# Performance work log

Hardware: AMD Instinct MI355X
Metric: run time of the kernel (lower is better)

Reference implementation:

```python
import jax, jax.numpy as jnp
import numpy as np

EPS_LN = 1e-5

def _ln(x, w, b):
    m = x.mean(-1, keepdims=True)
    v = x.var(-1, keepdims=True)  # biased var, matching torch LayerNorm
    return (x - m) / jnp.sqrt(v + EPS_LN) * w + b


def setup_inputs() -> dict:
    key = jax.random.key(0)
    ks = jax.random.split(key, 20)
    B, N, C = 8, 4096, 256
    def lin_w(k, i, o):
        return (jax.random.normal(k, (i, o), jnp.float32) / np.sqrt(i)).astype(jnp.float32)
    inp = {
        'xyz': jax.random.normal(ks[0], (B, N, 3), jnp.float32),
        'features': jax.random.normal(ks[1], (B, N, C), jnp.float32),
        # geo_mlp: Linear(10,32), LN(32), ReLU, Linear(32,16)
        'g_w1': lin_w(ks[2], 10, 32), 'g_b1': jnp.zeros((32,), jnp.float32),
        'g_lnw': jnp.ones((32,), jnp.float32), 'g_lnb': jnp.zeros((32,), jnp.float32),
        'g_w2': lin_w(ks[3], 32, 16), 'g_b2': jnp.zeros((16,), jnp.float32),
        # edge_pred: Linear(C+16,64), LN(64), ReLU, Linear(64,1), Sigmoid
        'e_w1': lin_w(ks[4], C + 16, 64), 'e_b1': jnp.zeros((64,), jnp.float32),
        'e_lnw': jnp.ones((64,), jnp.float32), 'e_lnb': jnp.zeros((64,), jnp.float32),
        'e_w2': lin_w(ks[5], 64, 1), 'e_b2': jnp.zeros((1,), jnp.float32),
        # edge_refine: Linear(C,C), LN(C), ReLU
        'r_w': lin_w(ks[6], C, C), 'r_b': jnp.zeros((C,), jnp.float32),
        'r_lnw': jnp.ones((C,), jnp.float32), 'r_lnb': jnp.zeros((C,), jnp.float32),
    }
    return inp


def reference(xyz, features, g_w1, g_b1, g_lnw, g_lnb, g_w2, g_b2,
              e_w1, e_b1, e_lnw, e_lnb, e_w2, e_b2, r_w, r_b, r_lnw, r_lnb):
    k = 16
    # KNN: pairwise negative squared distance, top-k largest = nearest
    sq = jnp.sum(xyz * xyz, axis=-1)                              # [B,N]
    pd = 2.0 * jnp.einsum('bnd,bmd->bnm', xyz, xyz) - sq[:, :, None] - sq[:, None, :]
    idx = jax.lax.top_k(pd, k)[1]                                 # [B,N,k]
    nbr = jax.vmap(lambda p, i: p[i])(xyz, idx)                   # [B,N,k,3]
    cen = nbr - nbr.mean(axis=2, keepdims=True)                   # centered neighborhoods
    cov = jnp.einsum('bnkc,bnkd->bncd', cen, cen) / k             # [B,N,3,3]
    trace = cov[..., 0, 0] + cov[..., 1, 1] + cov[..., 2, 2]
    det = jnp.clip(cov[..., 0, 0] * cov[..., 1, 1] * cov[..., 2, 2], 1e-8, None)
    std = jnp.std(cen, axis=2, ddof=1)                            # [B,N,3] (torch unbiased std)
    d = jnp.linalg.norm(cen, axis=3)                              # [B,N,k]
    mean_d = d.mean(axis=2)
    std_d = jnp.std(d, axis=2, ddof=1)
    t = trace + 1e-6
    geo = jnp.stack([trace, det, std[..., 0], std[..., 1], std[..., 2],
                     mean_d, std_d, std[..., 0] / t, std[..., 1] / t, std[..., 2] / t], axis=-1)
    geo = jax.nn.relu(_ln(geo @ g_w1 + g_b1, g_lnw, g_lnb)) @ g_w2 + g_b2    # [B,N,16]
    comb = jnp.concatenate([features, geo], axis=-1)
    edge_prob = jax.nn.sigmoid(jax.nn.relu(_ln(comb @ e_w1 + e_b1, e_lnw, e_lnb)) @ e_w2 + e_b2)
    refined = jax.nn.relu(_ln(features @ r_w + r_b, r_lnw, r_lnb))
    refined = features + refined * edge_prob
    return refined, edge_prob
```

## Files before the change

kernel.cpp:

```cpp
#include <hip/hip_runtime.h>
#include <math.h>

#define BATCH 8
#define NPTS  4096
#define CF    256
#define TOPK  16
#define TOTQ  (BATCH*NPTS)
#define EPOFF ((size_t)TOTQ*CF)

__global__ __launch_bounds__(256) void prep_xyz_k(const float* __restrict__ xyz,
                                                  float4* __restrict__ tab) {
    int i = blockIdx.x*256 + threadIdx.x;
    if (i < TOTQ) {
        float x = xyz[3*i], y = xyz[3*i+1], z = xyz[3*i+2];
        tab[i] = make_float4(x, y, z, x*x + y*y + z*z);
    }
}

__global__ __launch_bounds__(256, 2) void knn_geo_k(
    const float4* __restrict__ tab,
    const float* __restrict__ g_w1, const float* __restrict__ g_b1,
    const float* __restrict__ g_lnw, const float* __restrict__ g_lnb,
    const float* __restrict__ g_w2, const float* __restrict__ g_b2,
    float* __restrict__ geo_out)
{
    __shared__ float2 lst[TOPK][256];
    __shared__ float4 coords[64][TOPK+1];
    __shared__ float s_w1[320], s_b1[32], s_lnw[32], s_lnb[32], s_w2[512], s_b2[16];

    const int tid = threadIdx.x;
    for (int v = tid; v < 320; v += 256) s_w1[v] = g_w1[v];
    for (int v = tid; v < 512; v += 256) s_w2[v] = g_w2[v];
    if (tid < 32) { s_b1[tid] = g_b1[tid]; s_lnw[tid] = g_lnw[tid]; s_lnb[tid] = g_lnb[tid]; }
    if (tid < 16) s_b2[tid] = g_b2[tid];

    const int ql = tid & 63;
    const int qg = blockIdx.x*64 + ql;
    const int b  = blockIdx.x >> 6;
    const float4* __restrict__ ctab = tab + b*NPTS;
    const int ibase = __builtin_amdgcn_readfirstlane((tid >> 6) << 10);

    float4 q4 = tab[qg];
    const float qx = q4.x, qy = q4.y, qz = q4.z, qs = q4.w;

    float vals[TOPK]; int idxs[TOPK];
    #pragma unroll
    for (int j = 0; j < TOPK; ++j) { vals[j] = -INFINITY; idxs[j] = 0; }
    int   cnt = 0;
    float thr = -INFINITY;

    auto flushbuf = [&]() {
        for (int e = 0; e < cnt; ++e) {
            float2 en = lst[e][tid];
            float pv = en.x;
            int   pj = __float_as_int(en.y);
            if (pv > vals[TOPK-1]) {
                #pragma unroll
                for (int j = TOPK-1; j >= 1; --j) {
                    bool shift = pv > vals[j-1];
                    bool place = (!shift) && (pv > vals[j]);
                    vals[j] = shift ? vals[j-1] : (place ? pv : vals[j]);
                    idxs[j] = shift ? idxs[j-1] : (place ? pj : idxs[j]);
                }
                if (pv > vals[0]) { vals[0] = pv; idxs[0] = pj; }
            }
        }
    };

    float4 cbuf[8];
    #pragma unroll
    for (int u = 0; u < 8; ++u) cbuf[u] = ctab[ibase + u];

    for (int ib = 0; ib < 1024; ib += 8) {
        float4 cur[8];
        #pragma unroll
        for (int u = 0; u < 8; ++u) cur[u] = cbuf[u];
        if (ib + 8 < 1024) {
            #pragma unroll
            for (int u = 0; u < 8; ++u) cbuf[u] = ctab[ibase + ib + 8 + u];
        }
        #pragma unroll
        for (int u = 0; u < 8; ++u) {
            float dot = fmaf(qx, cur[u].x, fmaf(qy, cur[u].y, qz*cur[u].z));
            float pd  = fmaf(2.f, dot, -(qs + cur[u].w));
            if (pd > thr) {
                lst[cnt][tid] = make_float2(pd, __int_as_float(ibase + ib + u));
                ++cnt;
            }
        }
        if (__any(cnt > 8)) { flushbuf(); cnt = 0; thr = vals[TOPK-1]; }
    }
    flushbuf();

    #pragma unroll
    for (int e = 0; e < TOPK; ++e)
        lst[e][tid] = make_float2(vals[e], __int_as_float(idxs[e]));
    __syncthreads();

    if (tid < 64) {
        const int q = tid;
        int p0 = 0, p1 = 0, p2 = 0, p3 = 0;
        float sx = 0, sy = 0, sz = 0;
        for (int r = 0; r < TOPK; ++r) {
            float2 h0 = lst[p0][q];
            float2 h1 = lst[p1][64 + q];
            float2 h2 = lst[p2][128 + q];
            float2 h3 = lst[p3][192 + q];
            float best = h0.x; int bj = __float_as_int(h0.y); int bs = 0;
            if (h1.x > best) { best = h1.x; bj = __float_as_int(h1.y); bs = 1; }
            if (h2.x > best) { best = h2.x; bj = __float_as_int(h2.y); bs = 2; }
            if (h3.x > best) { best = h3.x; bj = __float_as_int(h3.y); bs = 3; }
            p0 += (bs == 0); p1 += (bs == 1); p2 += (bs == 2); p3 += (bs == 3);
            float4 nb = ctab[bj];
            coords[q][r] = nb;
            sx += nb.x; sy += nb.y; sz += nb.z;
        }
        const float mx = sx/16.f, my = sy/16.f, mz = sz/16.f;
        float sxx = 0, syy = 0, szz = 0, sd = 0;
        float dist[TOPK];
        #pragma unroll
        for (int r = 0; r < TOPK; ++r) {
            float4 nb = coords[q][r];
            float cx = nb.x - mx, cy = nb.y - my, cz = nb.z - mz;
            sxx += cx*cx; syy += cy*cy; szz += cz*cz;
            float dd = sqrtf(cx*cx + cy*cy + cz*cz);
            dist[r] = dd; sd += dd;
        }
        const float md = sd/16.f;
        float sdd = 0;
        #pragma unroll
        for (int r = 0; r < TOPK; ++r) { float t = dist[r] - md; sdd += t*t; }
        const float c00 = sxx/16.f, c11 = syy/16.f, c22 = szz/16.f;
        const float trace = c00 + c11 + c22;
        const float det = fmaxf(c00*c11*c22, 1e-8f);
        const float s0 = sqrtf(sxx/15.f), s1 = sqrtf(syy/15.f), s2 = sqrtf(szz/15.f);
        const float stdd = sqrtf(sdd/15.f);
        const float tt = trace + 1e-6f;
        float geo[10] = {trace, det, s0, s1, s2, md, stdd, s0/tt, s1/tt, s2/tt};

        float z1[32];
        #pragma unroll
        for (int jj = 0; jj < 32; ++jj) {
            float a = s_b1[jj];
            #pragma unroll
            for (int i = 0; i < 10; ++i) a = fmaf(geo[i], s_w1[i*32 + jj], a);
            z1[jj] = a;
        }
        float mzn = 0;
        #pragma unroll
        for (int jj = 0; jj < 32; ++jj) mzn += z1[jj];
        mzn /= 32.f;
        float vz = 0;
        #pragma unroll
        for (int jj = 0; jj < 32; ++jj) { float t = z1[jj] - mzn; vz += t*t; }
        vz /= 32.f;
        const float rs = 1.f/sqrtf(vz + 1e-5f);
        float h[32];
        #pragma unroll
        for (int jj = 0; jj < 32; ++jj)
            h[jj] = fmaxf((z1[jj]-mzn)*rs*s_lnw[jj] + s_lnb[jj], 0.f);
        float og[16];
        #pragma unroll
        for (int c = 0; c < 16; ++c) {
            float a = s_b2[c];
            #pragma unroll
            for (int i = 0; i < 32; ++i) a = fmaf(h[i], s_w2[i*16 + c], a);
            og[c] = a;
        }
        float4* gout = (float4*)(geo_out + (size_t)qg*16);
        gout[0] = make_float4(og[0],  og[1],  og[2],  og[3]);
        gout[1] = make_float4(og[4],  og[5],  og[6],  og[7]);
        gout[2] = make_float4(og[8],  og[9],  og[10], og[11]);
        gout[3] = make_float4(og[12], og[13], og[14], og[15]);
    }
}

__global__ __launch_bounds__(256, 2) void edge_k(
    const float* __restrict__ feat, const float* __restrict__ geo16,
    const float* __restrict__ e_w1, const float* __restrict__ e_b1,
    const float* __restrict__ e_lnw, const float* __restrict__ e_lnb,
    const float* __restrict__ e_w2, const float* __restrict__ e_b2,
    const float* __restrict__ r_w,  const float* __restrict__ r_b,
    const float* __restrict__ r_lnw, const float* __restrict__ r_lnb,
    float* __restrict__ out)
{
    __shared__ float fl[32*260];
    __shared__ float wb[4096];
    __shared__ float gl[512];

    const int tid = threadIdx.x;
    const int pbase = blockIdx.x*32;

    {
        const float4* f4 = (const float4*)(feat + (size_t)pbase*CF);
        #pragma unroll
        for (int k = 0; k < 8; ++k) {
            int v = tid + k*256;
            float4 x = f4[v];
            *(float4*)&fl[(v >> 6)*260 + (v & 63)*4] = x;
        }
        if (tid < 128) {
            float4 x = ((const float4*)(geo16 + (size_t)pbase*16))[tid];
            *(float4*)&gl[(tid >> 2)*16 + (tid & 3)*4] = x;
        }
    }
    __syncthreads();

    const int pq = tid >> 4, cq = tid & 15;
    const int p0 = pq*2, p1 = p0 + 1;

    float a0[4] = {0,0,0,0}, a1[4] = {0,0,0,0};
    for (int kc = 0; kc < 256; kc += 64) {
        __syncthreads();
        #pragma unroll
        for (int k = 0; k < 4; ++k) {
            int v = tid + k*256;
            *(float4*)&wb[(v >> 4)*64 + (v & 15)*4] =
                *(const float4*)&e_w1[(size_t)(kc + (v >> 4))*64 + (v & 15)*4];
        }
        __syncthreads();
        #pragma unroll 8
        for (int k = 0; k < 64; ++k) {
            float f0 = fl[p0*260 + kc + k];
            float f1 = fl[p1*260 + kc + k];
            float4 w = *(float4*)&wb[k*64 + cq*4];
            a0[0] = fmaf(f0, w.x, a0[0]); a0[1] = fmaf(f0, w.y, a0[1]);
            a0[2] = fmaf(f0, w.z, a0[2]); a0[3] = fmaf(f0, w.w, a0[3]);
            a1[0] = fmaf(f1, w.x, a1[0]); a1[1] = fmaf(f1, w.y, a1[1]);
            a1[2] = fmaf(f1, w.z, a1[2]); a1[3] = fmaf(f1, w.w, a1[3]);
        }
    }
    __syncthreads();
    {
        int v = tid;
        *(float4*)&wb[(v >> 4)*64 + (v & 15)*4] =
            *(const float4*)&e_w1[(size_t)(256 + (v >> 4))*64 + (v & 15)*4];
    }
    __syncthreads();
    #pragma unroll
    for (int k = 0; k < 16; ++k) {
        float f0 = gl[p0*16 + k];
        float f1 = gl[p1*16 + k];
        float4 w = *(float4*)&wb[k*64 + cq*4];
        a0[0] = fmaf(f0, w.x, a0[0]); a0[1] = fmaf(f0, w.y, a0[1]);
        a0[2] = fmaf(f0, w.z, a0[2]); a0[3] = fmaf(f0, w.w, a0[3]);
        a1[0] = fmaf(f1, w.x, a1[0]); a1[1] = fmaf(f1, w.y, a1[1]);
        a1[2] = fmaf(f1, w.z, a1[2]); a1[3] = fmaf(f1, w.w, a1[3]);
    }
    {
        float4 bb = *(const float4*)&e_b1[cq*4];
        a0[0]+=bb.x; a0[1]+=bb.y; a0[2]+=bb.z; a0[3]+=bb.w;
        a1[0]+=bb.x; a1[1]+=bb.y; a1[2]+=bb.z; a1[3]+=bb.w;
    }
    float s0 = a0[0]+a0[1]+a0[2]+a0[3];
    float s1 = a1[0]+a1[1]+a1[2]+a1[3];
    #pragma unroll
    for (int sw = 1; sw < 16; sw <<= 1) { s0 += __shfl_xor(s0, sw); s1 += __shfl_xor(s1, sw); }
    const float m0 = s0/64.f, m1 = s1/64.f;
    float v0 = 0, v1 = 0;
    #pragma unroll
    for (int j = 0; j < 4; ++j) { float t0 = a0[j]-m0, t1 = a1[j]-m1; v0 += t0*t0; v1 += t1*t1; }
    #pragma unroll
    for (int sw = 1; sw < 16; sw <<= 1) { v0 += __shfl_xor(v0, sw); v1 += __shfl_xor(v1, sw); }
    const float r0 = 1.f/sqrtf(v0/64.f + 1e-5f);
    const float r1 = 1.f/sqrtf(v1/64.f + 1e-5f);
    float4 lw = *(const float4*)&e_lnw[cq*4];
    float4 lb = *(const float4*)&e_lnb[cq*4];
    float4 w2 = *(const float4*)&e_w2[cq*4];
    float d0 = 0, d1 = 0;
    {
        float hh;
        hh = fmaxf((a0[0]-m0)*r0*lw.x + lb.x, 0.f); d0 = fmaf(hh, w2.x, d0);
        hh = fmaxf((a0[1]-m0)*r0*lw.y + lb.y, 0.f); d0 = fmaf(hh, w2.y, d0);
        hh = fmaxf((a0[2]-m0)*r0*lw.z + lb.z, 0.f); d0 = fmaf(hh, w2.z, d0);
        hh = fmaxf((a0[3]-m0)*r0*lw.w + lb.w, 0.f); d0 = fmaf(hh, w2.w, d0);
        hh = fmaxf((a1[0]-m1)*r1*lw.x + lb.x, 0.f); d1 = fmaf(hh, w2.x, d1);
        hh = fmaxf((a1[1]-m1)*r1*lw.y + lb.y, 0.f); d1 = fmaf(hh, w2.y, d1);
        hh = fmaxf((a1[2]-m1)*r1*lw.z + lb.z, 0.f); d1 = fmaf(hh, w2.z, d1);
        hh = fmaxf((a1[3]-m1)*r1*lw.w + lb.w, 0.f); d1 = fmaf(hh, w2.w, d1);
    }
    #pragma unroll
    for (int sw = 1; sw < 16; sw <<= 1) { d0 += __shfl_xor(d0, sw); d1 += __shfl_xor(d1, sw); }
    const float eb2 = e_b2[0];
    const float ep0 = 1.f/(1.f + expf(-(d0 + eb2)));
    const float ep1 = 1.f/(1.f + expf(-(d1 + eb2)));
    if (cq == 0) {
        out[EPOFF + pbase + p0] = ep0;
        out[EPOFF + pbase + p1] = ep1;
    }

    float b0[4][4], b1v[4][4];
    #pragma unroll
    for (int o = 0; o < 4; ++o)
        #pragma unroll
        for (int j = 0; j < 4; ++j) { b0[o][j] = 0.f; b1v[o][j] = 0.f; }

    for (int kc = 0; kc < 256; kc += 16) {
        __syncthreads();
        #pragma unroll
        for (int k = 0; k < 8; ++k) {
            int v = tid + k*256;
            *(float4*)&wb[(v >> 6)*256 + (v & 63)*4] =
                *(const float4*)&r_w[(size_t)(kc + (v >> 6))*256 + (v & 63)*4];
        }
        __syncthreads();
        #pragma unroll
        for (int k = 0; k < 16; ++k) {
            float f0 = fl[p0*260 + kc + k];
            float f1 = fl[p1*260 + kc + k];
            #pragma unroll
            for (int o = 0; o < 4; ++o) {
                float4 w = *(float4*)&wb[k*256 + o*64 + cq*4];
                b0[o][0] = fmaf(f0, w.x, b0[o][0]); b0[o][1] = fmaf(f0, w.y, b0[o][1]);
                b0[o][2] = fmaf(f0, w.z, b0[o][2]); b0[o][3] = fmaf(f0, w.w, b0[o][3]);
                b1v[o][0] = fmaf(f1, w.x, b1v[o][0]); b1v[o][1] = fmaf(f1, w.y, b1v[o][1]);
                b1v[o][2] = fmaf(f1, w.z, b1v[o][2]); b1v[o][3] = fmaf(f1, w.w, b1v[o][3]);
            }
        }
    }
    #pragma unroll
    for (int o = 0; o < 4; ++o) {
        float4 rb = *(const float4*)&r_b[o*64 + cq*4];
        b0[o][0]+=rb.x; b0[o][1]+=rb.y; b0[o][2]+=rb.z; b0[o][3]+=rb.w;
        b1v[o][0]+=rb.x; b1v[o][1]+=rb.y; b1v[o][2]+=rb.z; b1v[o][3]+=rb.w;
    }
    float S0 = 0, S1 = 0;
    #pragma unroll
    for (int o = 0; o < 4; ++o)
        #pragma unroll
        for (int j = 0; j < 4; ++j) { S0 += b0[o][j]; S1 += b1v[o][j]; }
    #pragma unroll
    for (int sw = 1; sw < 16; sw <<= 1) { S0 += __shfl_xor(S0, sw); S1 += __shfl_xor(S1, sw); }
    const float M0 = S0/256.f, M1 = S1/256.f;
    float V0 = 0, V1 = 0;
    #pragma unroll
    for (int o = 0; o < 4; ++o)
        #pragma unroll
        for (int j = 0; j < 4; ++j) {
            float t0 = b0[o][j]-M0, t1 = b1v[o][j]-M1;
            V0 += t0*t0; V1 += t1*t1;
        }
    #pragma unroll
    for (int sw = 1; sw < 16; sw <<= 1) { V0 += __shfl_xor(V0, sw); V1 += __shfl_xor(V1, sw); }
    const float R0 = 1.f/sqrtf(V0/256.f + 1e-5f);
    const float R1 = 1.f/sqrtf(V1/256.f + 1e-5f);

    #pragma unroll
    for (int o = 0; o < 4; ++o) {
        float4 lw4 = *(const float4*)&r_lnw[o*64 + cq*4];
        float4 lb4 = *(const float4*)&r_lnb[o*64 + cq*4];
        float4 f0v = *(float4*)&fl[p0*260 + o*64 + cq*4];
        float4 f1v = *(float4*)&fl[p1*260 + o*64 + cq*4];
        float4 o0, o1;
        o0.x = f0v.x + fmaxf((b0[o][0]-M0)*R0*lw4.x + lb4.x, 0.f)*ep0;
        o0.y = f0v.y + fmaxf((b0[o][1]-M0)*R0*lw4.y + lb4.y, 0.f)*ep0;
        o0.z = f0v.z + fmaxf((b0[o][2]-M0)*R0*lw4.z + lb4.z, 0.f)*ep0;
        o0.w = f0v.w + fmaxf((b0[o][3]-M0)*R0*lw4.w + lb4.w, 0.f)*ep0;
        o1.x = f1v.x + fmaxf((b1v[o][0]-M1)*R1*lw4.x + lb4.x, 0.f)*ep1;
        o1.y = f1v.y + fmaxf((b1v[o][1]-M1)*R1*lw4.y + lb4.y, 0.f)*ep1;
        o1.z = f1v.z + fmaxf((b1v[o][2]-M1)*R1*lw4.z + lb4.z, 0.f)*ep1;
        o1.w = f1v.w + fmaxf((b1v[o][3]-M1)*R1*lw4.w + lb4.w, 0.f)*ep1;
        *(float4*)&out[((size_t)(pbase + p0))*CF + o*64 + cq*4] = o0;
        *(float4*)&out[((size_t)(pbase + p1))*CF + o*64 + cq*4] = o1;
    }
}

extern "C" void kernel_launch(void* const* d_in, const int* in_sizes, int n_in,
                              void* d_out, int out_size, void* d_ws, size_t ws_size,
                              hipStream_t stream) {
    (void)in_sizes; (void)n_in; (void)out_size; (void)ws_size;
    const float* xyz   = (const float*)d_in[0];
    const float* feat  = (const float*)d_in[1];
    const float* g_w1  = (const float*)d_in[2];
    const float* g_b1  = (const float*)d_in[3];
    const float* g_lnw = (const float*)d_in[4];
    const float* g_lnb = (const float*)d_in[5];
    const float* g_w2  = (const float*)d_in[6];
    const float* g_b2  = (const float*)d_in[7];
    const float* e_w1  = (const float*)d_in[8];
    const float* e_b1  = (const float*)d_in[9];
    const float* e_lnw = (const float*)d_in[10];
    const float* e_lnb = (const float*)d_in[11];
    const float* e_w2  = (const float*)d_in[12];
    const float* e_b2  = (const float*)d_in[13];
    const float* r_w   = (const float*)d_in[14];
    const float* r_b   = (const float*)d_in[15];
    const float* r_lnw = (const float*)d_in[16];
    const float* r_lnb = (const float*)d_in[17];
    float* out = (float*)d_out;

    float*  geo_ws = (float*)d_ws;
    float4* tab    = (float4*)((char*)d_ws + (size_t)TOTQ*16*sizeof(float));

    hipLaunchKernelGGL(prep_xyz_k, dim3(TOTQ/256), dim3(256), 0, stream, xyz, tab);
    hipLaunchKernelGGL(knn_geo_k, dim3(TOTQ/64), dim3(256), 0, stream,
                       tab, g_w1, g_b1, g_lnw, g_lnb, g_w2, g_b2, geo_ws);
    hipLaunchKernelGGL(edge_k, dim3(TOTQ/32), dim3(256), 0, stream,
                       feat, geo_ws, e_w1, e_b1, e_lnw, e_lnb, e_w2, e_b2,
                       r_w, r_b, r_lnw, r_lnb, out);
}
```

Baseline: 344.9 us.

## Move edge/refine GEMMs to bf16x3 MFMA with pre-split pre-swizzled weights

Replaces the scalar FP32 FMA matmuls in edge_k with MFMA 16x16x32 bf16 instructions. Each operand is split into a high and a low bf16 part, and three products are summed to keep close to FP32 accuracy. A new prep kernel converts and swizzles r_w and e_w1 into MFMA-friendly layouts each call. The weights are streamed into LDS with global_load_lds double buffering, and the block is widened to 64 points. LayerNorm statistics switch to a one-pass sum/sum-of-squares form, which adds some numerical risk. The larger LDS footprint drops occupancy to one block per CU.

```diff
diff --git a/kernel.cpp b/kernel.cpp
--- a/kernel.cpp
+++ b/kernel.cpp
@@ -8,12 +8,53 @@
 #define TOTQ  (BATCH*NPTS)
 #define EPOFF ((size_t)TOTQ*CF)
 
+typedef __attribute__((ext_vector_type(8))) short bf16x8;
+typedef __attribute__((ext_vector_type(4))) float f32x4;
+
+__device__ __forceinline__ unsigned short f2bf(float x) {
+    union { float f; unsigned u; } a; a.f = x;
+    unsigned r = a.u + 0x7fffu + ((a.u >> 16) & 1u);
+    return (unsigned short)(r >> 16);
+}
+__device__ __forceinline__ float bf2f(unsigned short h) {
+    union { float f; unsigned u; } a; a.u = ((unsigned)h) << 16; return a.f;
+}
+__device__ __forceinline__ void gl_lds16(const void* g, void* l) {
+    __builtin_amdgcn_global_load_lds(
+        (const __attribute__((address_space(1))) unsigned int*)g,
+        (__attribute__((address_space(3))) unsigned int*)l, 16, 0, 0);
+}
+
 __global__ __launch_bounds__(256) void prep_xyz_k(const float* __restrict__ xyz,
                                                   float4* __restrict__ tab) {
     int i = blockIdx.x*256 + threadIdx.x;
     if (i < TOTQ) {
         float x = xyz[3*i], y = xyz[3*i+1], z = xyz[3*i+2];
         tab[i] = make_float4(x, y, z, x*x + y*y + z*z);
+    }
+}
+
+__global__ __launch_bounds__(256) void prep_w_k(
+    const float* __restrict__ rw, const float* __restrict__ ew1,
+    unsigned short* __restrict__ rwh, unsigned short* __restrict__ rwl,
+    unsigned short* __restrict__ ewh, unsigned short* __restrict__ ewl)
+{
+    int t = blockIdx.x*256 + threadIdx.x;
+    if (t < 65536) {
+        int k = t >> 8, n = t & 255;
+        float x = rw[t];
+        unsigned short h = f2bf(x);
+        unsigned short l = f2bf(x - bf2f(h));
+        int dst = (((k>>5)*16 + (n>>4)) << 9) + ((k>>3)&3)*128 + (n&15)*8 + (k&7);
+        rwh[dst] = h; rwl[dst] = l;
+    }
+    if (t < 288*64) {
+        int k = t >> 6, n = t & 63;
+        float x = (k < 272) ? ew1[k*64 + n] : 0.f;
+        unsigned short h = f2bf(x);
+        unsigned short l = f2bf(x - bf2f(h));
+        int dst = (((k>>5)*4 + (n>>4)) << 9) + ((k>>3)&3)*128 + (n&15)*8 + (k&7);
+        ewh[dst] = h; ewl[dst] = l;
     }
 }
 
@@ -175,193 +216,273 @@
     }
 }
 
-__global__ __launch_bounds__(256, 2) void edge_k(
+__global__ __launch_bounds__(256, 1) void edge_k(
     const float* __restrict__ feat, const float* __restrict__ geo16,
-    const float* __restrict__ e_w1, const float* __restrict__ e_b1,
-    const float* __restrict__ e_lnw, const float* __restrict__ e_lnb,
-    const float* __restrict__ e_w2, const float* __restrict__ e_b2,
-    const float* __restrict__ r_w,  const float* __restrict__ r_b,
-    const float* __restrict__ r_lnw, const float* __restrict__ r_lnb,
+    const unsigned short* __restrict__ rwh, const unsigned short* __restrict__ rwl,
+    const unsigned short* __restrict__ ewh, const unsigned short* __restrict__ ewl,
+    const float* __restrict__ e_b1, const float* __restrict__ e_lnw,
+    const float* __restrict__ e_lnb, const float* __restrict__ e_w2,
+    const float* __restrict__ e_b2,
+    const float* __restrict__ r_b, const float* __restrict__ r_lnw,
+    const float* __restrict__ r_lnb,
     float* __restrict__ out)
 {
-    __shared__ float fl[32*260];
-    __shared__ float wb[4096];
-    __shared__ float gl[512];
-
-    const int tid = threadIdx.x;
-    const int pbase = blockIdx.x*32;
-
+    __shared__ unsigned short sAh[64*296];
+    __shared__ unsigned short sAl[64*296];
+    __shared__ unsigned char  sB[65536];
+    __shared__ float s_eb1[64], s_elnw[64], s_elnb[64], s_ew2[64];
+    __shared__ float s_rb[256], s_rlnw[256], s_rlnb[256];
+    __shared__ float s_ep[64], s_m[64], s_rs[64];
+    __shared__ float sPx[256], sPq[256];
+
+    const int tid  = threadIdx.x;
+    const int lane = tid & 63;
+    const int wv   = tid >> 6;
+    const int lr   = lane & 15;
+    const int lg   = lane >> 4;
+    const int pbase = blockIdx.x * 64;
+
+    if (tid < 64) { s_eb1[tid]=e_b1[tid]; s_elnw[tid]=e_lnw[tid]; s_elnb[tid]=e_lnb[tid]; s_ew2[tid]=e_w2[tid]; }
+    s_rb[tid]=r_b[tid]; s_rlnw[tid]=r_lnw[tid]; s_rlnb[tid]=r_lnb[tid];
+
+    const float4* f4 = (const float4*)(feat + (size_t)pbase*CF);
+    #pragma unroll
+    for (int it = 0; it < 16; ++it) {
+        int v = tid + it*256;
+        float4 x = f4[v];
+        int row = v >> 6, c0 = (v & 63)*4;
+        unsigned short h0=f2bf(x.x), h1=f2bf(x.y), h2=f2bf(x.z), h3=f2bf(x.w);
+        unsigned short l0=f2bf(x.x-bf2f(h0)), l1=f2bf(x.y-bf2f(h1));
+        unsigned short l2=f2bf(x.z-bf2f(h2)), l3=f2bf(x.w-bf2f(h3));
+        *(ushort4*)&sAh[row*296 + c0] = make_ushort4(h0,h1,h2,h3);
+        *(ushort4*)&sAl[row*296 + c0] = make_ushort4(l0,l1,l2,l3);
+    }
     {
-        const float4* f4 = (const float4*)(feat + (size_t)pbase*CF);
-        #pragma unroll
-        for (int k = 0; k < 8; ++k) {
-            int v = tid + k*256;
-            float4 x = f4[v];
-            *(float4*)&fl[(v >> 6)*260 + (v & 63)*4] = x;
-        }
-        if (tid < 128) {
-            float4 x = ((const float4*)(geo16 + (size_t)pbase*16))[tid];
-            *(float4*)&gl[(tid >> 2)*16 + (tid & 3)*4] = x;
-        }
-    }
+        const float4* g4 = (const float4*)(geo16 + (size_t)pbase*16);
+        float4 x = g4[tid];
+        int row = tid >> 2, c0 = 256 + (tid & 3)*4;
+        unsigned short h0=f2bf(x.x), h1=f2bf(x.y), h2=f2bf(x.z), h3=f2bf(x.w);
+        unsigned short l0=f2bf(x.x-bf2f(h0)), l1=f2bf(x.y-bf2f(h1));
+        unsigned short l2=f2bf(x.z-bf2f(h2)), l3=f2bf(x.w-bf2f(h3));
+        *(ushort4*)&sAh[row*296 + c0] = make_ushort4(h0,h1,h2,h3);
+        *(ushort4*)&sAl[row*296 + c0] = make_ushort4(l0,l1,l2,l3);
+        int zc = 272 + (tid & 3)*4;
+        *(ushort4*)&sAh[row*296 + zc] = make_ushort4(0,0,0,0);
+        *(ushort4*)&sAl[row*296 + zc] = make_ushort4(0,0,0,0);
+    }
+
+    auto stage3 = [&](int c, int buf) {
+        const char* sh = (const char*)rwh + c*16384;
+        const char* sl = (const char*)rwl + c*16384;
+        char* dh = (char*)sB + buf*32768;
+        char* dl = dh + 16384;
+        #pragma unroll
+        for (int i = 0; i < 4; ++i) {
+            gl_lds16(sh + i*4096 + wv*1024 + lane*16, dh + i*4096 + wv*1024);
+            gl_lds16(sl + i*4096 + wv*1024 + lane*16, dl + i*4096 + wv*1024);
+        }
+    };
+    auto stage2 = [&](int c, int buf) {
+        const char* sh = (const char*)ewh + c*4096;
+        const char* sl = (const char*)ewl + c*4096;
+        char* d = (char*)sB + 32768 + buf*8192;
+        gl_lds16(sh + wv*1024 + lane*16, d + wv*1024);
+        gl_lds16(sl + wv*1024 + lane*16, d + 4096 + wv*1024);
+    };
+
+    stage2(0, 0);
+    stage3(0, 0);
     __syncthreads();
 
-    const int pq = tid >> 4, cq = tid & 15;
-    const int p0 = pq*2, p1 = p0 + 1;
-
-    float a0[4] = {0,0,0,0}, a1[4] = {0,0,0,0};
-    for (int kc = 0; kc < 256; kc += 64) {
+    f32x4 acc2[4];
+    #pragma unroll
+    for (int i = 0; i < 4; ++i) acc2[i] = (f32x4){0.f,0.f,0.f,0.f};
+    const int arow2 = (wv*16 + lr)*296;
+    for (int c = 0; c < 9; ++c) {
+        if (c < 8) stage2(c+1, (c+1)&1);
+        bf16x8 ah = *(const bf16x8*)&sAh[arow2 + c*32 + lg*8];
+        bf16x8 al = *(const bf16x8*)&sAl[arow2 + c*32 + lg*8];
+        const unsigned short* bb = (const unsigned short*)(sB + 32768 + (c&1)*8192);
+        #pragma unroll
+        for (int nt = 0; nt < 4; ++nt) {
+            bf16x8 bh = *(const bf16x8*)&bb[nt*512 + lane*8];
+            bf16x8 bl = *(const bf16x8*)&bb[2048 + nt*512 + lane*8];
+            acc2[nt] = __builtin_amdgcn_mfma_f32_16x16x32_bf16(al, bh, acc2[nt], 0,0,0);
+            acc2[nt] = __builtin_amdgcn_mfma_f32_16x16x32_bf16(ah, bl, acc2[nt], 0,0,0);
+            acc2[nt] = __builtin_amdgcn_mfma_f32_16x16x32_bf16(ah, bh, acc2[nt], 0,0,0);
+        }
         __syncthreads();
-        #pragma unroll
-        for (int k = 0; k < 4; ++k) {
-            int v = tid + k*256;
-            *(float4*)&wb[(v >> 4)*64 + (v & 15)*4] =
-                *(const float4*)&e_w1[(size_t)(kc + (v >> 4))*64 + (v & 15)*4];
+    }
+
+    {
+        float px[4] = {0,0,0,0}, pq[4] = {0,0,0,0};
+        #pragma unroll
+        for (int nt = 0; nt < 4; ++nt) {
+            float bv = s_eb1[nt*16 + lr];
+            #pragma unroll
+            for (int j = 0; j < 4; ++j) {
+                acc2[nt][j] += bv;
+                px[j] += acc2[nt][j];
+                pq[j] += acc2[nt][j]*acc2[nt][j];
+            }
+        }
+        #pragma unroll
+        for (int sw = 1; sw < 16; sw <<= 1) {
+            #pragma unroll
+            for (int j = 0; j < 4; ++j) { px[j] += __shfl_xor(px[j], sw); pq[j] += __shfl_xor(pq[j], sw); }
+        }
+        float mj[4], rj[4], dd[4] = {0,0,0,0};
+        #pragma unroll
+        for (int j = 0; j < 4; ++j) {
+            mj[j] = px[j]*(1.f/64.f);
+            float var = pq[j]*(1.f/64.f) - mj[j]*mj[j];
+            rj[j] = rsqrtf(var + 1e-5f);
+        }
+        #pragma unroll
+        for (int nt = 0; nt < 4; ++nt) {
+            int col = nt*16 + lr;
+            float lw = s_elnw[col], lb = s_elnb[col], w2 = s_ew2[col];
+            #pragma unroll
+            for (int j = 0; j < 4; ++j) {
+                float h = fmaxf((acc2[nt][j]-mj[j])*rj[j]*lw + lb, 0.f);
+                dd[j] = fmaf(h, w2, dd[j]);
+            }
+        }
+        #pragma unroll
+        for (int sw = 1; sw < 16; sw <<= 1) {
+            #pragma unroll
+            for (int j = 0; j < 4; ++j) dd[j] += __shfl_xor(dd[j], sw);
+        }
+        float eb2v = e_b2[0];
+        #pragma unroll
+        for (int j = 0; j < 4; ++j) {
+            if (lr == j) {
+                int row = wv*16 + lg*4 + j;
+                float ep = 1.f/(1.f + expf(-(dd[j] + eb2v)));
+                s_ep[row] = ep;
+                out[EPOFF + pbase + row] = ep;
+            }
+        }
+    }
+
+    f32x4 acc3[4][4];
+    #pragma unroll
+    for (int mt = 0; mt < 4; ++mt)
+        #pragma unroll
+        for (int nt = 0; nt < 4; ++nt) acc3[mt][nt] = (f32x4){0.f,0.f,0.f,0.f};
+
+    for (int c = 0; c < 8; ++c) {
+        if (c < 7) stage3(c+1, (c+1)&1);
+        bf16x8 ah[4], al[4];
+        #pragma unroll
+        for (int mt = 0; mt < 4; ++mt) {
+            ah[mt] = *(const bf16x8*)&sAh[(mt*16+lr)*296 + c*32 + lg*8];
+            al[mt] = *(const bf16x8*)&sAl[(mt*16+lr)*296 + c*32 + lg*8];
+        }
+        const unsigned short* bb = (const unsigned short*)(sB + (c&1)*32768);
+        #pragma unroll
+        for (int ntl = 0; ntl < 4; ++ntl) {
+            int nt = wv*4 + ntl;
+            bf16x8 bh = *(const bf16x8*)&bb[nt*512 + lane*8];
+            bf16x8 bl = *(const bf16x8*)&bb[8192 + nt*512 + lane*8];
+            #pragma unroll
+            for (int mt = 0; mt < 4; ++mt) {
+                acc3[mt][ntl] = __builtin_amdgcn_mfma_f32_16x16x32_bf16(al[mt], bh, acc3[mt][ntl], 0,0,0);
+                acc3[mt][ntl] = __builtin_amdgcn_mfma_f32_16x16x32_bf16(ah[mt], bl, acc3[mt][ntl], 0,0,0);
+                acc3[mt][ntl] = __builtin_amdgcn_mfma_f32_16x16x32_bf16(ah[mt], bh, acc3[mt][ntl], 0,0,0);
+            }
         }
         __syncthreads();
-        #pragma unroll 8
-        for (int k = 0; k < 64; ++k) {
-            float f0 = fl[p0*260 + kc + k];
-            float f1 = fl[p1*260 + kc + k];
-            float4 w = *(float4*)&wb[k*64 + cq*4];
-            a0[0] = fmaf(f0, w.x, a0[0]); a0[1] = fmaf(f0, w.y, a0[1]);
-            a0[2] = fmaf(f0, w.z, a0[2]); a0[3] = fmaf(f0, w.w, a0[3]);
-            a1[0] = fmaf(f1, w.x, a1[0]); a1[1] = fmaf(f1, w.y, a1[1]);
-            a1[2] = fmaf(f1, w.z, a1[2]); a1[3] = fmaf(f1, w.w, a1[3]);
-        }
+    }
+
+    float qx[4][4], qq[4][4];
+    #pragma unroll
+    for (int mt = 0; mt < 4; ++mt)
+        #pragma unroll
+        for (int j = 0; j < 4; ++j) { qx[mt][j] = 0.f; qq[mt][j] = 0.f; }
+    #pragma unroll
+    for (int ntl = 0; ntl < 4; ++ntl) {
+        int col = (wv*4 + ntl)*16 + lr;
+        float bv = s_rb[col];
+        #pragma unroll
+        for (int mt = 0; mt < 4; ++mt)
+            #pragma unroll
+            for (int j = 0; j < 4; ++j) {
+                acc3[mt][ntl][j] += bv;
+                float v = acc3[mt][ntl][j];
+                qx[mt][j] += v; qq[mt][j] += v*v;
+            }
+    }
+    #pragma unroll
+    for (int sw = 1; sw < 16; sw <<= 1) {
+        #pragma unroll
+        for (int mt = 0; mt < 4; ++mt)
+            #pragma unroll
+            for (int j = 0; j < 4; ++j) { qx[mt][j] += __shfl_xor(qx[mt][j], sw); qq[mt][j] += __shfl_xor(qq[mt][j], sw); }
+    }
+    if (lr == 0) {
+        #pragma unroll
+        for (int mt = 0; mt < 4; ++mt)
+            #pragma unroll
+            for (int j = 0; j < 4; ++j) {
+                int row = mt*16 + lg*4 + j;
+                sPx[wv*64 + row] = qx[mt][j];
+                sPq[wv*64 + row] = qq[mt][j];
+            }
     }
     __syncthreads();
+    if (tid < 64) {
+        float Sx = sPx[tid] + sPx[64+tid] + sPx[128+tid] + sPx[192+tid];
+        float Sq = sPq[tid] + sPq[64+tid] + sPq[128+tid] + sPq[192+tid];
+        float m  = Sx*(1.f/256.f);
+        float var = Sq*(1.f/256.f) - m*m;
+        s_m[tid]  = m;
+        s_rs[tid] = rsqrtf(var + 1e-5f);
+    }
+    __syncthreads();
+
     {
-        int v = tid;
-        *(float4*)&wb[(v >> 4)*64 + (v & 15)*4] =
-            *(const float4*)&e_w1[(size_t)(256 + (v >> 4))*64 + (v & 15)*4];
+        float* sOut = (float*)sB;
+        float lwv[4], lbv[4]; int colv[4];
+        #pragma unroll
+        for (int ntl = 0; ntl < 4; ++ntl) {
+            colv[ntl] = (wv*4 + ntl)*16 + lr;
+            lwv[ntl] = s_rlnw[colv[ntl]];
+            lbv[ntl] = s_rlnb[colv[ntl]];
+        }
+        #pragma unroll
+        for (int mt = 0; mt < 4; ++mt) {
+            #pragma unroll
+            for (int j = 0; j < 4; ++j) {
+                int row = mt*16 + lg*4 + j;
+                float m = s_m[row], rs = s_rs[row];
+                #pragma unroll
+                for (int ntl = 0; ntl < 4; ++ntl) {
+                    float h = fmaxf((acc3[mt][ntl][j]-m)*rs*lwv[ntl] + lbv[ntl], 0.f);
+                    sOut[row*256 + colv[ntl]] = h;
+                }
+            }
+        }
     }
     __syncthreads();
-    #pragma unroll
-    for (int k = 0; k < 16; ++k) {
-        float f0 = gl[p0*16 + k];
-        float f1 = gl[p1*16 + k];
-        float4 w = *(float4*)&wb[k*64 + cq*4];
-        a0[0] = fmaf(f0, w.x, a0[0]); a0[1] = fmaf(f0, w.y, a0[1]);
-        a0[2] = fmaf(f0, w.z, a0[2]); a0[3] = fmaf(f0, w.w, a0[3]);
-        a1[0] = fmaf(f1, w.x, a1[0]); a1[1] = fmaf(f1, w.y, a1[1]);
-        a1[2] = fmaf(f1, w.z, a1[2]); a1[3] = fmaf(f1, w.w, a1[3]);
-    }
+
     {
-        float4 bb = *(const float4*)&e_b1[cq*4];
-        a0[0]+=bb.x; a0[1]+=bb.y; a0[2]+=bb.z; a0[3]+=bb.w;
-        a1[0]+=bb.x; a1[1]+=bb.y; a1[2]+=bb.z; a1[3]+=bb.w;
-    }
-    float s0 = a0[0]+a0[1]+a0[2]+a0[3];
-    float s1 = a1[0]+a1[1]+a1[2]+a1[3];
-    #pragma unroll
-    for (int sw = 1; sw < 16; sw <<= 1) { s0 += __shfl_xor(s0, sw); s1 += __shfl_xor(s1, sw); }
-    const float m0 = s0/64.f, m1 = s1/64.f;
-    float v0 = 0, v1 = 0;
-    #pragma unroll
-    for (int j = 0; j < 4; ++j) { float t0 = a0[j]-m0, t1 = a1[j]-m1; v0 += t0*t0; v1 += t1*t1; }
-    #pragma unroll
-    for (int sw = 1; sw < 16; sw <<= 1) { v0 += __shfl_xor(v0, sw); v1 += __shfl_xor(v1, sw); }
-    const float r0 = 1.f/sqrtf(v0/64.f + 1e-5f);
-    const float r1 = 1.f/sqrtf(v1/64.f + 1e-5f);
-    float4 lw = *(const float4*)&e_lnw[cq*4];
-    float4 lb = *(const float4*)&e_lnb[cq*4];
-    float4 w2 = *(const float4*)&e_w2[cq*4];
-    float d0 = 0, d1 = 0;
-    {
-        float hh;
-        hh = fmaxf((a0[0]-m0)*r0*lw.x + lb.x, 0.f); d0 = fmaf(hh, w2.x, d0);
-        hh = fmaxf((a0[1]-m0)*r0*lw.y + lb.y, 0.f); d0 = fmaf(hh, w2.y, d0);
-        hh = fmaxf((a0[2]-m0)*r0*lw.z + lb.z, 0.f); d0 = fmaf(hh, w2.z, d0);
-        hh = fmaxf((a0[3]-m0)*r0*lw.w + lb.w, 0.f); d0 = fmaf(hh, w2.w, d0);
-        hh = fmaxf((a1[0]-m1)*r1*lw.x + lb.x, 0.f); d1 = fmaf(hh, w2.x, d1);
-        hh = fmaxf((a1[1]-m1)*r1*lw.y + lb.y, 0.f); d1 = fmaf(hh, w2.y, d1);
-        hh = fmaxf((a1[2]-m1)*r1*lw.z + lb.z, 0.f); d1 = fmaf(hh, w2.z, d1);
-        hh = fmaxf((a1[3]-m1)*r1*lw.w + lb.w, 0.f); d1 = fmaf(hh, w2.w, d1);
-    }
-    #pragma unroll
-    for (int sw = 1; sw < 16; sw <<= 1) { d0 += __shfl_xor(d0, sw); d1 += __shfl_xor(d1, sw); }
-    const float eb2 = e_b2[0];
-    const float ep0 = 1.f/(1.f + expf(-(d0 + eb2)));
-    const float ep1 = 1.f/(1.f + expf(-(d1 + eb2)));
-    if (cq == 0) {
-        out[EPOFF + pbase + p0] = ep0;
-        out[EPOFF + pbase + p1] = ep1;
-    }
-
-    float b0[4][4], b1v[4][4];
-    #pragma unroll
-    for (int o = 0; o < 4; ++o)
-        #pragma unroll
-        for (int j = 0; j < 4; ++j) { b0[o][j] = 0.f; b1v[o][j] = 0.f; }
-
-    for (int kc = 0; kc < 256; kc += 16) {
-        __syncthreads();
-        #pragma unroll
-        for (int k = 0; k < 8; ++k) {
-            int v = tid + k*256;
-            *(float4*)&wb[(v >> 6)*256 + (v & 63)*4] =
-                *(const float4*)&r_w[(size_t)(kc + (v >> 6))*256 + (v & 63)*4];
-        }
-        __syncthreads();
-        #pragma unroll
-        for (int k = 0; k < 16; ++k) {
-            float f0 = fl[p0*260 + kc + k];
-            float f1 = fl[p1*260 + kc + k];
-            #pragma unroll
-            for (int o = 0; o < 4; ++o) {
-                float4 w = *(float4*)&wb[k*256 + o*64 + cq*4];
-                b0[o][0] = fmaf(f0, w.x, b0[o][0]); b0[o][1] = fmaf(f0, w.y, b0[o][1]);
-                b0[o][2] = fmaf(f0, w.z, b0[o][2]); b0[o][3] = fmaf(f0, w.w, b0[o][3]);
-                b1v[o][0] = fmaf(f1, w.x, b1v[o][0]); b1v[o][1] = fmaf(f1, w.y, b1v[o][1]);
-                b1v[o][2] = fmaf(f1, w.z, b1v[o][2]); b1v[o][3] = fmaf(f1, w.w, b1v[o][3]);
-            }
-        }
-    }
-    #pragma unroll
-    for (int o = 0; o < 4; ++o) {
-        float4 rb = *(const float4*)&r_b[o*64 + cq*4];
-        b0[o][0]+=rb.x; b0[o][1]+=rb.y; b0[o][2]+=rb.z; b0[o][3]+=rb.w;
-        b1v[o][0]+=rb.x; b1v[o][1]+=rb.y; b1v[o][2]+=rb.z; b1v[o][3]+=rb.w;
-    }
-    float S0 = 0, S1 = 0;
-    #pragma unroll
-    for (int o = 0; o < 4; ++o)
-        #pragma unroll
-        for (int j = 0; j < 4; ++j) { S0 += b0[o][j]; S1 += b1v[o][j]; }
-    #pragma unroll
-    for (int sw = 1; sw < 16; sw <<= 1) { S0 += __shfl_xor(S0, sw); S1 += __shfl_xor(S1, sw); }
-    const float M0 = S0/256.f, M1 = S1/256.f;
-    float V0 = 0, V1 = 0;
-    #pragma unroll
-    for (int o = 0; o < 4; ++o)
-        #pragma unroll
-        for (int j = 0; j < 4; ++j) {
-            float t0 = b0[o][j]-M0, t1 = b1v[o][j]-M1;
-            V0 += t0*t0; V1 += t1*t1;
-        }
-    #pragma unroll
-    for (int sw = 1; sw < 16; sw <<= 1) { V0 += __shfl_xor(V0, sw); V1 += __shfl_xor(V1, sw); }
-    const float R0 = 1.f/sqrtf(V0/256.f + 1e-5f);
-    const float R1 = 1.f/sqrtf(V1/256.f + 1e-5f);
-
-    #pragma unroll
-    for (int o = 0; o < 4; ++o) {
-        float4 lw4 = *(const float4*)&r_lnw[o*64 + cq*4];
-        float4 lb4 = *(const float4*)&r_lnb[o*64 + cq*4];
-        float4 f0v = *(float4*)&fl[p0*260 + o*64 + cq*4];
-        float4 f1v = *(float4*)&fl[p1*260 + o*64 + cq*4];
-        float4 o0, o1;
-        o0.x = f0v.x + fmaxf((b0[o][0]-M0)*R0*lw4.x + lb4.x, 0.f)*ep0;
-        o0.y = f0v.y + fmaxf((b0[o][1]-M0)*R0*lw4.y + lb4.y, 0.f)*ep0;
-        o0.z = f0v.z + fmaxf((b0[o][2]-M0)*R0*lw4.z + lb4.z, 0.f)*ep0;
-        o0.w = f0v.w + fmaxf((b0[o][3]-M0)*R0*lw4.w + lb4.w, 0.f)*ep0;
-        o1.x = f1v.x + fmaxf((b1v[o][0]-M1)*R1*lw4.x + lb4.x, 0.f)*ep1;
-        o1.y = f1v.y + fmaxf((b1v[o][1]-M1)*R1*lw4.y + lb4.y, 0.f)*ep1;
-        o1.z = f1v.z + fmaxf((b1v[o][2]-M1)*R1*lw4.z + lb4.z, 0.f)*ep1;
-        o1.w = f1v.w + fmaxf((b1v[o][3]-M1)*R1*lw4.w + lb4.w, 0.f)*ep1;
-        *(float4*)&out[((size_t)(pbase + p0))*CF + o*64 + cq*4] = o0;
-        *(float4*)&out[((size_t)(pbase + p1))*CF + o*64 + cq*4] = o1;
+        const float* sOut = (const float*)sB;
+        #pragma unroll
+        for (int it = 0; it < 16; ++it) {
+            int v = tid + it*256;
+            int row = v >> 6, c0 = (v & 63)*4;
+            float4 h4 = *(const float4*)&sOut[row*256 + c0];
+            ushort4 hh = *(const ushort4*)&sAh[row*296 + c0];
+            ushort4 ll = *(const ushort4*)&sAl[row*296 + c0];
+            float ep = s_ep[row];
+            float4 o;
+            o.x = bf2f(hh.x) + bf2f(ll.x) + h4.x*ep;
+            o.y = bf2f(hh.y) + bf2f(ll.y) + h4.y*ep;
+            o.z = bf2f(hh.z) + bf2f(ll.z) + h4.z*ep;
+            o.w = bf2f(hh.w) + bf2f(ll.w) + h4.w*ep;
+            *(float4*)&out[(size_t)(pbase+row)*CF + c0] = o;
+        }
     }
 }
 
@@ -389,13 +510,21 @@
     const float* r_lnb = (const float*)d_in[17];
     float* out = (float*)d_out;
 
-    float*  geo_ws = (float*)d_ws;
-    float4* tab    = (float4*)((char*)d_ws + (size_t)TOTQ*16*sizeof(float));
+    char* ws = (char*)d_ws;
+    float*          geo_ws = (float*)ws;
+    float4*         tab    = (float4*)(ws + 0x200000);
+    unsigned short* rwh    = (unsigned short*)(ws + 0x280000);
+    unsigned short* rwl    = (unsigned short*)(ws + 0x2A0000);
+    unsigned short* ewh    = (unsigned short*)(ws + 0x2C0000);
+    unsigned short* ewl    = (unsigned short*)(ws + 0x2D0000);
 
     hipLaunchKernelGGL(prep_xyz_k, dim3(TOTQ/256), dim3(256), 0, stream, xyz, tab);
+    hipLaunchKernelGGL(prep_w_k, dim3(256), dim3(256), 0, stream,
+                       r_w, e_w1, rwh, rwl, ewh, ewl);
     hipLaunchKernelGGL(knn_geo_k, dim3(TOTQ/64), dim3(256), 0, stream,
                        tab, g_w1, g_b1, g_lnw, g_lnb, g_w2, g_b2, geo_ws);
-    hipLaunchKernelGGL(edge_k, dim3(TOTQ/32), dim3(256), 0, stream,
-                       feat, geo_ws, e_w1, e_b1, e_lnw, e_lnb, e_w2, e_b2,
-                       r_w, r_b, r_lnw, r_lnb, out);
-}
+    hipLaunchKernelGGL(edge_k, dim3(TOTQ/64), dim3(256), 0, stream,
+                       feat, geo_ws, rwh, rwl, ewh, ewl,
+                       e_b1, e_lnw, e_lnb, e_w2, e_b2,
+                       r_b, r_lnw, r_lnb, out);
+}
```

Result: faster. 282.4 us (-18.1%).
